# Kernel optimization log

Hardware: AMD Instinct MI355X
Metric: run time of the kernel (lower is better)

Reference implementation:

```python
import jax, jax.numpy as jnp
import numpy as np

B, T, E, H = 4, 4096, 1024, 64

def setup_inputs() -> dict:
    key = jax.random.key(0)
    k1, k2, k3, k4 = jax.random.split(key, 4)
    embeddings = jax.random.normal(k1, (B, T, E), dtype=jnp.float32)
    Wq = jax.random.normal(k2, (H, E), dtype=jnp.float32) * (1.0 / np.sqrt(E))
    Wk = jax.random.normal(k3, (H, E), dtype=jnp.float32) * (1.0 / np.sqrt(E))
    Wv = jax.random.normal(k4, (H, E), dtype=jnp.float32) * (1.0 / np.sqrt(E))
    return {"embeddings": embeddings, "Wq": Wq, "Wk": Wk, "Wv": Wv}

def reference(embeddings, Wq, Wk, Wv):
    # Linear(E, H, bias=False): x @ W.T, W: [H, E]
    q = jnp.einsum('bte,he->bth', embeddings, Wq)  # [B,T,H]
    k = jnp.einsum('bte,he->bth', embeddings, Wk)  # [B,T,H]
    v = jnp.einsum('bte,he->bth', embeddings, Wv)  # [B,T,H]
    scale = embeddings.shape[-1] ** -0.5  # NOTE: source scales by embed_size**-0.5
    wei = jnp.einsum('bqh,bkh->bqk', q, k) * scale  # [B,T,T]
    Tn = embeddings.shape[1]
    causal = jnp.tril(jnp.ones((Tn, Tn), dtype=bool))
    wei = jnp.where(causal[None, :, :], wei, -jnp.inf)
    wei = jax.nn.softmax(wei, axis=-1)
    return jnp.einsum('bqk,bkh->bqh', wei, v)  # [B,T,H]
```

## Files before the change

kernel.cpp:

```cpp
#include <hip/hip_runtime.h>
#include <math.h>
#include <stdint.h>

#define BN 4
#define TN 4096
#define EN 1024
#define HN 64
#define BT (BN*TN)

typedef __attribute__((ext_vector_type(8))) short   short8;
typedef __attribute__((ext_vector_type(4))) float   f32x4;
typedef __attribute__((ext_vector_type(4))) unsigned short us4;
typedef __attribute__((ext_vector_type(8))) unsigned short us8;

__device__ __forceinline__ unsigned short f2b(float f) {
    union { float f; uint32_t u; } v; v.f = f;
    uint32_t u = v.u;
    return (unsigned short)((u + 0x7FFFu + ((u >> 16) & 1u)) >> 16);
}

__device__ __forceinline__ float fexp2(float x) {
#if __has_builtin(__builtin_amdgcn_exp2f)
    return __builtin_amdgcn_exp2f(x);
#else
    return exp2f(x);
#endif
}

__global__ __launch_bounds__(256)
void wconv(const float* __restrict__ Wq, const float* __restrict__ Wk,
           const float* __restrict__ Wv, unsigned short* __restrict__ W16) {
    const int row = blockIdx.x;
    const int t = threadIdx.x;
    const float* src;
    float sc = 1.0f;
    if (row < 64)       { src = Wq + (size_t)row * EN; sc = 0.045084220f; }
    else if (row < 128) { src = Wk + (size_t)(row - 64) * EN; }
    else                { src = Wv + (size_t)(row - 128) * EN; }
    float4 v = *(const float4*)(src + t * 4);
    us4 p;
    p[0] = f2b(v.x * sc); p[1] = f2b(v.y * sc);
    p[2] = f2b(v.z * sc); p[3] = f2b(v.w * sc);
    *(us4*)&W16[(size_t)row * EN + t * 4] = p;
}

__global__ __launch_bounds__(512, 2)
void qkv_gemm(const float* __restrict__ emb, const unsigned short* __restrict__ W16,
              unsigned short* __restrict__ QK, unsigned short* __restrict__ VT) {
    __shared__ __align__(16) unsigned short A_lds[2][64][72];
    __shared__ __align__(16) unsigned short B_lds[2][192][72];

    const int tid = threadIdx.x;
    const int wid = tid >> 6, lane = tid & 63;
    const int c = lane & 15, g = lane >> 4;
    const int wm = wid & 1, wn = wid >> 1;
    const int r0 = blockIdx.x * 64;

    const int ar = tid >> 3, ach = tid & 7;

    const f32x4 fzero = {0.f, 0.f, 0.f, 0.f};
    f32x4 acc[2][3];
    #pragma unroll
    for (int i = 0; i < 2; ++i)
        #pragma unroll
        for (int j = 0; j < 3; ++j) acc[i][j] = fzero;

    {
        float4 a0 = *(const float4*)&emb[(size_t)(r0 + ar) * EN + ach * 8];
        float4 a1 = *(const float4*)&emb[(size_t)(r0 + ar) * EN + ach * 8 + 4];
        us8 ap;
        ap[0] = f2b(a0.x); ap[1] = f2b(a0.y); ap[2] = f2b(a0.z); ap[3] = f2b(a0.w);
        ap[4] = f2b(a1.x); ap[5] = f2b(a1.y); ap[6] = f2b(a1.z); ap[7] = f2b(a1.w);
        *(us8*)&A_lds[0][ar][ach * 8] = ap;
        #pragma unroll
        for (int s = 0; s < 3; ++s) {
            const int f = tid + 512 * s;
            const int br = f >> 3, bch = f & 7;
            *(us8*)&B_lds[0][br][bch * 8] = *(const us8*)&W16[(size_t)br * EN + bch * 8];
        }
    }
    __syncthreads();

    for (int t = 0; t < 16; ++t) {
        const int cur = t & 1;
        const bool pf = (t < 15);
        const int kn = (t + 1) * 64;

        float4 a0, a1;
        us8 bw0, bw1, bw2;
        if (pf) {
            a0 = *(const float4*)&emb[(size_t)(r0 + ar) * EN + kn + ach * 8];
            a1 = *(const float4*)&emb[(size_t)(r0 + ar) * EN + kn + ach * 8 + 4];
            bw0 = *(const us8*)&W16[(size_t)((tid +    0) >> 3) * EN + kn + (tid & 7) * 8];
            bw1 = *(const us8*)&W16[(size_t)((tid +  512) >> 3) * EN + kn + ((tid + 512) & 7) * 8];
            bw2 = *(const us8*)&W16[(size_t)((tid + 1024) >> 3) * EN + kn + ((tid + 1024) & 7) * 8];
        }

        short8 af[2][2], bf[3][2];
        #pragma unroll
        for (int rt = 0; rt < 2; ++rt)
            #pragma unroll
            for (int ks = 0; ks < 2; ++ks)
                af[rt][ks] = *(const short8*)&A_lds[cur][32 * wm + 16 * rt + c][32 * ks + 8 * g];
        #pragma unroll
        for (int nt = 0; nt < 3; ++nt)
            #pragma unroll
            for (int ks = 0; ks < 2; ++ks)
                bf[nt][ks] = *(const short8*)&B_lds[cur][48 * wn + 16 * nt + c][32 * ks + 8 * g];
        #pragma unroll
        for (int ks = 0; ks < 2; ++ks)
            #pragma unroll
            for (int rt = 0; rt < 2; ++rt)
                #pragma unroll
                for (int nt = 0; nt < 3; ++nt)
                    acc[rt][nt] = __builtin_amdgcn_mfma_f32_16x16x32_bf16(
                        af[rt][ks], bf[nt][ks], acc[rt][nt], 0, 0, 0);

        if (pf) {
            us8 ap;
            ap[0] = f2b(a0.x); ap[1] = f2b(a0.y); ap[2] = f2b(a0.z); ap[3] = f2b(a0.w);
            ap[4] = f2b(a1.x); ap[5] = f2b(a1.y); ap[6] = f2b(a1.z); ap[7] = f2b(a1.w);
            *(us8*)&A_lds[cur ^ 1][ar][ach * 8] = ap;
            *(us8*)&B_lds[cur ^ 1][(tid +    0) >> 3][((tid +    0) & 7) * 8] = bw0;
            *(us8*)&B_lds[cur ^ 1][(tid +  512) >> 3][((tid +  512) & 7) * 8] = bw1;
            *(us8*)&B_lds[cur ^ 1][(tid + 1024) >> 3][((tid + 1024) & 7) * 8] = bw2;
        }
        __syncthreads();
    }

    #pragma unroll
    for (int rt = 0; rt < 2; ++rt) {
        #pragma unroll
        for (int nt = 0; nt < 3; ++nt) {
            const int n = 48 * wn + 16 * nt + c;
            const int wsel = n >> 6;
            const int d = n & 63;
            const int rbase = r0 + 32 * wm + 16 * rt + 4 * g;
            if (wsel < 2) {
                #pragma unroll
                for (int j = 0; j < 4; ++j)
                    QK[(size_t)wsel * BT * HN + (size_t)(rbase + j) * HN + d] =
                        f2b(acc[rt][nt][j]);
            } else {
                const int bb = rbase >> 12;
                const int tt = rbase & 4095;
                us4 p;
                #pragma unroll
                for (int j = 0; j < 4; ++j) p[j] = f2b(acc[rt][nt][j]);
                *(us4*)&VT[(size_t)bb * HN * TN + (size_t)d * TN + tt] = p;
            }
        }
    }
}

#define NW 4

__global__ __launch_bounds__(256, 2)
void attn(const unsigned short* __restrict__ QK,
          const unsigned short* __restrict__ VT, float* __restrict__ out) {
    __shared__ __align__(16) unsigned short KV[NW][2][64][72];
    __shared__ __align__(16) float MLm[NW][32];
    __shared__ __align__(16) float MLl[NW][32];
    __shared__ __align__(16) float ML2m[32];
    __shared__ __align__(16) float ML2l[32];

    const int tid = threadIdx.x;
    const int w = tid >> 6, lane = tid & 63, c = lane & 15, g = lane >> 4;
    const int bid = blockIdx.x;
    const int b = bid & 3;
    const int qt = (TN / 32 - 1) - (bid >> 2);

    const unsigned short* Qg = QK + ((size_t)b * TN + (size_t)qt * 32) * HN;
    const unsigned short* Kg = QK + (size_t)BT * HN + (size_t)b * TN * HN;
    const unsigned short* Vg = VT + (size_t)b * HN * TN;

    short8 bq[2][2];
    #pragma unroll
    for (int ct = 0; ct < 2; ++ct)
        #pragma unroll
        for (int ks = 0; ks < 2; ++ks)
            bq[ct][ks] = *(const short8*)&Qg[(size_t)(16 * ct + c) * HN + 32 * ks + 8 * g];

    const f32x4 fzero = {0.f, 0.f, 0.f, 0.f};
    f32x4 o[2][4];
    #pragma unroll
    for (int i = 0; i < 2; ++i)
        #pragma unroll
        for (int j = 0; j < 4; ++j) o[i][j] = fzero;
    float m[2] = {-INFINITY, -INFINITY};
    float l[2] = {0.f, 0.f};

    const int jmax = qt >> 1;
    unsigned short* Ks = &KV[w][0][0][0];
    unsigned short* Vs = &KV[w][1][0][0];

    for (int jt = w; jt <= jmax; jt += NW) {
        #pragma unroll
        for (int i = 0; i < 8; ++i) {
            const int f = lane + 64 * i;
            const int r = f >> 3, ch = f & 7;
            *(us8*)&Ks[r * 72 + ch * 8] =
                *(const us8*)&Kg[((size_t)jt * 64 + r) * HN + ch * 8];
        }
        #pragma unroll
        for (int i = 0; i < 8; ++i) {
            const int f = lane + 64 * i;
            const int r = f >> 3, ch = f & 7;
            *(us8*)&Vs[r * 72 + ch * 8] =
                *(const us8*)&Vg[(size_t)r * TN + (size_t)jt * 64 + ch * 8];
        }

        f32x4 st[4][2];
        #pragma unroll
        for (int kt = 0; kt < 4; ++kt)
            #pragma unroll
            for (int ct = 0; ct < 2; ++ct) st[kt][ct] = fzero;
        #pragma unroll
        for (int kt = 0; kt < 4; ++kt) {
            #pragma unroll
            for (int ks = 0; ks < 2; ++ks) {
                short8 ak = *(const short8*)&Ks[(16 * kt + c) * 72 + 32 * ks + 8 * g];
                #pragma unroll
                for (int ct = 0; ct < 2; ++ct)
                    st[kt][ct] = __builtin_amdgcn_mfma_f32_16x16x32_bf16(
                        ak, bq[ct][ks], st[kt][ct], 0, 0, 0);
            }
        }

        if (jt == jmax) {
            const int koff = jt * 64 - qt * 32;
            #pragma unroll
            for (int kt = 0; kt < 4; ++kt)
                #pragma unroll
                for (int ct = 0; ct < 2; ++ct)
                    #pragma unroll
                    for (int j = 0; j < 4; ++j)
                        if (16 * kt + 4 * g + j + koff > 16 * ct + c)
                            st[kt][ct][j] = -INFINITY;
        }

        #pragma unroll
        for (int ct = 0; ct < 2; ++ct) {
            float pmax = -INFINITY;
            #pragma unroll
            for (int kt = 0; kt < 4; ++kt)
                #pragma unroll
                for (int j = 0; j < 4; ++j) pmax = fmaxf(pmax, st[kt][ct][j]);
            pmax = fmaxf(pmax, __shfl_xor(pmax, 16));
            pmax = fmaxf(pmax, __shfl_xor(pmax, 32));
            const float mn = fmaxf(m[ct], pmax);
            const float alpha = fexp2(m[ct] - mn);
            float ls = 0.f;
            #pragma unroll
            for (int kt = 0; kt < 4; ++kt)
                #pragma unroll
                for (int j = 0; j < 4; ++j) {
                    float p = fexp2(st[kt][ct][j] - mn);
                    st[kt][ct][j] = p;
                    ls += p;
                }
            ls += __shfl_xor(ls, 16);
            ls += __shfl_xor(ls, 32);
            l[ct] = l[ct] * alpha + ls;
            m[ct] = mn;

            float a4[4];
            #pragma unroll
            for (int j = 0; j < 4; ++j) a4[j] = __shfl(alpha, 4 * g + j);
            #pragma unroll
            for (int dt = 0; dt < 4; ++dt)
                #pragma unroll
                for (int j = 0; j < 4; ++j) o[ct][dt][j] *= a4[j];
        }

        #pragma unroll
        for (int kt = 0; kt < 4; ++kt)
            #pragma unroll
            for (int ct = 0; ct < 2; ++ct) {
                us4 p;
                #pragma unroll
                for (int j = 0; j < 4; ++j) p[j] = f2b(st[kt][ct][j]);
                *(us4*)&Ks[(16 * ct + c) * 72 + 16 * kt + 4 * g] = p;
            }

        #pragma unroll
        for (int ks = 0; ks < 2; ++ks) {
            short8 pa[2];
            #pragma unroll
            for (int qp = 0; qp < 2; ++qp)
                pa[qp] = *(const short8*)&Ks[(16 * qp + c) * 72 + 32 * ks + 8 * g];
            #pragma unroll
            for (int dt = 0; dt < 4; ++dt) {
                short8 bv = *(const short8*)&Vs[(16 * dt + c) * 72 + 32 * ks + 8 * g];
                #pragma unroll
                for (int qp = 0; qp < 2; ++qp)
                    o[qp][dt] = __builtin_amdgcn_mfma_f32_16x16x32_bf16(
                        pa[qp], bv, o[qp][dt], 0, 0, 0);
            }
        }
    }

    if (g == 0) {
        MLm[w][c]      = m[0];  MLl[w][c]      = l[0];
        MLm[w][c + 16] = m[1];  MLl[w][c + 16] = l[1];
    }
    __syncthreads();

    if (tid < 32) {
        const int q = tid;
        float M = MLm[0][q];
        #pragma unroll
        for (int s = 1; s < NW; ++s) M = fmaxf(M, MLm[s][q]);
        float L = 0.f;
        #pragma unroll
        for (int s = 0; s < NW; ++s) L += MLl[s][q] * fexp2(MLm[s][q] - M);
        ML2m[q] = M;
        ML2l[q] = L;
    }
    __syncthreads();

    float* Oslab = (float*)&KV[0][0][0][0];
    float* Ow = Oslab + w * (32 * 65);
    #pragma unroll
    for (int qp = 0; qp < 2; ++qp) {
        float mo[4];
        #pragma unroll
        for (int j = 0; j < 4; ++j) mo[j] = __shfl(m[qp], 4 * g + j);
        #pragma unroll
        for (int j = 0; j < 4; ++j) {
            const int q = 16 * qp + 4 * g + j;
            const float sc = fexp2(mo[j] - ML2m[q]);
            #pragma unroll
            for (int dt = 0; dt < 4; ++dt)
                Ow[q * 65 + 16 * dt + c] = o[qp][dt][j] * sc;
        }
    }
    __syncthreads();

    const int d = 16 * w + c;
    #pragma unroll
    for (int tq = 0; tq < 8; ++tq) {
        const int q = 4 * tq + g;
        float v = 0.f;
        #pragma unroll
        for (int s = 0; s < NW; ++s) v += Oslab[s * (32 * 65) + q * 65 + d];
        out[((size_t)b * TN + (size_t)qt * 32 + q) * HN + d] = v / ML2l[q];
    }
}

extern "C" void kernel_launch(void* const* d_in, const int* in_sizes, int n_in,
                              void* d_out, int out_size, void* d_ws, size_t ws_size,
                              hipStream_t stream) {
    const float* emb = (const float*)d_in[0];
    const float* Wq  = (const float*)d_in[1];
    const float* Wk  = (const float*)d_in[2];
    const float* Wv  = (const float*)d_in[3];
    float* out = (float*)d_out;

    unsigned short* ws  = (unsigned short*)d_ws;
    unsigned short* W16 = ws;
    unsigned short* QK  = ws + 196608;
    unsigned short* VT  = ws + 196608 + 2 * (size_t)BT * HN;

    wconv<<<192, 256, 0, stream>>>(Wq, Wk, Wv, W16);
    qkv_gemm<<<BT / 64, 512, 0, stream>>>(emb, W16, QK, VT);
    attn<<<BN * (TN / 32), 256, 0, stream>>>(QK, VT, out);
}
```

Before: 144.2 us.

## Deepen GEMM prefetch, double attention waves, read K/V fragments directly

The QKV GEMM now keeps two K-steps of global loads in flight in register double buffers, with the loop unrolled by two, instead of one. The attention kernel goes from 4 to 8 waves per block, splitting the key tiles across more waves. It drops the per-wave LDS staging of K and V and loads MFMA operand fragments straight from global memory; LDS is kept only for the P tile and the final cross-wave reduction. This cuts LDS traffic and footprint so more blocks can be resident, at the cost of uncoalesced global fragment loads, a larger cross-wave merge and higher register pressure.

```diff
diff --git a/kernel.cpp b/kernel.cpp
--- a/kernel.cpp
+++ b/kernel.cpp
@@ -55,8 +55,11 @@
     const int c = lane & 15, g = lane >> 4;
     const int wm = wid & 1, wn = wid >> 1;
     const int r0 = blockIdx.x * 64;
-
     const int ar = tid >> 3, ach = tid & 7;
+
+    const int br0 = tid >> 3,           bch0 = tid & 7;
+    const int br1 = (tid + 512) >> 3,   bch1 = bch0;
+    const int br2 = (tid + 1024) >> 3,  bch2 = bch0;
 
     const f32x4 fzero = {0.f, 0.f, 0.f, 0.f};
     f32x4 acc[2][3];
@@ -65,35 +68,39 @@
         #pragma unroll
         for (int j = 0; j < 3; ++j) acc[i][j] = fzero;
 
+    float4 pa0[2], pa1[2];
+    us8 pb0[2], pb1[2], pb2[2];
+
+    #pragma unroll
+    for (int t = 0; t < 2; ++t) {
+        const int k0 = t * 64;
+        pa0[t] = *(const float4*)&emb[(size_t)(r0 + ar) * EN + k0 + ach * 8];
+        pa1[t] = *(const float4*)&emb[(size_t)(r0 + ar) * EN + k0 + ach * 8 + 4];
+        pb0[t] = *(const us8*)&W16[(size_t)br0 * EN + k0 + bch0 * 8];
+        pb1[t] = *(const us8*)&W16[(size_t)br1 * EN + k0 + bch1 * 8];
+        pb2[t] = *(const us8*)&W16[(size_t)br2 * EN + k0 + bch2 * 8];
+    }
     {
-        float4 a0 = *(const float4*)&emb[(size_t)(r0 + ar) * EN + ach * 8];
-        float4 a1 = *(const float4*)&emb[(size_t)(r0 + ar) * EN + ach * 8 + 4];
         us8 ap;
-        ap[0] = f2b(a0.x); ap[1] = f2b(a0.y); ap[2] = f2b(a0.z); ap[3] = f2b(a0.w);
-        ap[4] = f2b(a1.x); ap[5] = f2b(a1.y); ap[6] = f2b(a1.z); ap[7] = f2b(a1.w);
+        ap[0] = f2b(pa0[0].x); ap[1] = f2b(pa0[0].y); ap[2] = f2b(pa0[0].z); ap[3] = f2b(pa0[0].w);
+        ap[4] = f2b(pa1[0].x); ap[5] = f2b(pa1[0].y); ap[6] = f2b(pa1[0].z); ap[7] = f2b(pa1[0].w);
         *(us8*)&A_lds[0][ar][ach * 8] = ap;
-        #pragma unroll
-        for (int s = 0; s < 3; ++s) {
-            const int f = tid + 512 * s;
-            const int br = f >> 3, bch = f & 7;
-            *(us8*)&B_lds[0][br][bch * 8] = *(const us8*)&W16[(size_t)br * EN + bch * 8];
-        }
+        *(us8*)&B_lds[0][br0][bch0 * 8] = pb0[0];
+        *(us8*)&B_lds[0][br1][bch1 * 8] = pb1[0];
+        *(us8*)&B_lds[0][br2][bch2 * 8] = pb2[0];
     }
     __syncthreads();
 
+    #pragma unroll 2
     for (int t = 0; t < 16; ++t) {
         const int cur = t & 1;
-        const bool pf = (t < 15);
-        const int kn = (t + 1) * 64;
-
-        float4 a0, a1;
-        us8 bw0, bw1, bw2;
-        if (pf) {
-            a0 = *(const float4*)&emb[(size_t)(r0 + ar) * EN + kn + ach * 8];
-            a1 = *(const float4*)&emb[(size_t)(r0 + ar) * EN + kn + ach * 8 + 4];
-            bw0 = *(const us8*)&W16[(size_t)((tid +    0) >> 3) * EN + kn + (tid & 7) * 8];
-            bw1 = *(const us8*)&W16[(size_t)((tid +  512) >> 3) * EN + kn + ((tid + 512) & 7) * 8];
-            bw2 = *(const us8*)&W16[(size_t)((tid + 1024) >> 3) * EN + kn + ((tid + 1024) & 7) * 8];
+        if (t + 2 < 16) {
+            const int kn = (t + 2) * 64;
+            pa0[cur] = *(const float4*)&emb[(size_t)(r0 + ar) * EN + kn + ach * 8];
+            pa1[cur] = *(const float4*)&emb[(size_t)(r0 + ar) * EN + kn + ach * 8 + 4];
+            pb0[cur] = *(const us8*)&W16[(size_t)br0 * EN + kn + bch0 * 8];
+            pb1[cur] = *(const us8*)&W16[(size_t)br1 * EN + kn + bch1 * 8];
+            pb2[cur] = *(const us8*)&W16[(size_t)br2 * EN + kn + bch2 * 8];
         }
 
         short8 af[2][2], bf[3][2];
@@ -116,14 +123,15 @@
                     acc[rt][nt] = __builtin_amdgcn_mfma_f32_16x16x32_bf16(
                         af[rt][ks], bf[nt][ks], acc[rt][nt], 0, 0, 0);
 
-        if (pf) {
+        if (t + 1 < 16) {
+            const int nb = cur ^ 1;
             us8 ap;
-            ap[0] = f2b(a0.x); ap[1] = f2b(a0.y); ap[2] = f2b(a0.z); ap[3] = f2b(a0.w);
-            ap[4] = f2b(a1.x); ap[5] = f2b(a1.y); ap[6] = f2b(a1.z); ap[7] = f2b(a1.w);
-            *(us8*)&A_lds[cur ^ 1][ar][ach * 8] = ap;
-            *(us8*)&B_lds[cur ^ 1][(tid +    0) >> 3][((tid +    0) & 7) * 8] = bw0;
-            *(us8*)&B_lds[cur ^ 1][(tid +  512) >> 3][((tid +  512) & 7) * 8] = bw1;
-            *(us8*)&B_lds[cur ^ 1][(tid + 1024) >> 3][((tid + 1024) & 7) * 8] = bw2;
+            ap[0] = f2b(pa0[nb].x); ap[1] = f2b(pa0[nb].y); ap[2] = f2b(pa0[nb].z); ap[3] = f2b(pa0[nb].w);
+            ap[4] = f2b(pa1[nb].x); ap[5] = f2b(pa1[nb].y); ap[6] = f2b(pa1[nb].z); ap[7] = f2b(pa1[nb].w);
+            *(us8*)&A_lds[nb][ar][ach * 8] = ap;
+            *(us8*)&B_lds[nb][br0][bch0 * 8] = pb0[nb];
+            *(us8*)&B_lds[nb][br1][bch1 * 8] = pb1[nb];
+            *(us8*)&B_lds[nb][br2][bch2 * 8] = pb2[nb];
         }
         __syncthreads();
     }
@@ -153,12 +161,12 @@
     }
 }
 
-#define NW 4
-
-__global__ __launch_bounds__(256, 2)
+#define NW 8
+
+__global__ __launch_bounds__(512, 4)
 void attn(const unsigned short* __restrict__ QK,
           const unsigned short* __restrict__ VT, float* __restrict__ out) {
-    __shared__ __align__(16) unsigned short KV[NW][2][64][72];
+    __shared__ __align__(16) unsigned char SLAB[NW * 32 * 65 * 4];
     __shared__ __align__(16) float MLm[NW][32];
     __shared__ __align__(16) float MLl[NW][32];
     __shared__ __align__(16) float ML2m[32];
@@ -174,6 +182,8 @@
     const unsigned short* Kg = QK + (size_t)BT * HN + (size_t)b * TN * HN;
     const unsigned short* Vg = VT + (size_t)b * HN * TN;
 
+    unsigned short* Pw = (unsigned short*)SLAB + (size_t)w * 32 * 72;
+
     short8 bq[2][2];
     #pragma unroll
     for (int ct = 0; ct < 2; ++ct)
@@ -191,25 +201,8 @@
     float l[2] = {0.f, 0.f};
 
     const int jmax = qt >> 1;
-    unsigned short* Ks = &KV[w][0][0][0];
-    unsigned short* Vs = &KV[w][1][0][0];
 
     for (int jt = w; jt <= jmax; jt += NW) {
-        #pragma unroll
-        for (int i = 0; i < 8; ++i) {
-            const int f = lane + 64 * i;
-            const int r = f >> 3, ch = f & 7;
-            *(us8*)&Ks[r * 72 + ch * 8] =
-                *(const us8*)&Kg[((size_t)jt * 64 + r) * HN + ch * 8];
-        }
-        #pragma unroll
-        for (int i = 0; i < 8; ++i) {
-            const int f = lane + 64 * i;
-            const int r = f >> 3, ch = f & 7;
-            *(us8*)&Vs[r * 72 + ch * 8] =
-                *(const us8*)&Vg[(size_t)r * TN + (size_t)jt * 64 + ch * 8];
-        }
-
         f32x4 st[4][2];
         #pragma unroll
         for (int kt = 0; kt < 4; ++kt)
@@ -219,7 +212,8 @@
         for (int kt = 0; kt < 4; ++kt) {
             #pragma unroll
             for (int ks = 0; ks < 2; ++ks) {
-                short8 ak = *(const short8*)&Ks[(16 * kt + c) * 72 + 32 * ks + 8 * g];
+                short8 ak = *(const short8*)
+                    &Kg[((size_t)jt * 64 + 16 * kt + c) * HN + 32 * ks + 8 * g];
                 #pragma unroll
                 for (int ct = 0; ct < 2; ++ct)
                     st[kt][ct] = __builtin_amdgcn_mfma_f32_16x16x32_bf16(
@@ -280,7 +274,7 @@
                 us4 p;
                 #pragma unroll
                 for (int j = 0; j < 4; ++j) p[j] = f2b(st[kt][ct][j]);
-                *(us4*)&Ks[(16 * ct + c) * 72 + 16 * kt + 4 * g] = p;
+                *(us4*)&Pw[(16 * ct + c) * 72 + 16 * kt + 4 * g] = p;
             }
 
         #pragma unroll
@@ -288,10 +282,11 @@
             short8 pa[2];
             #pragma unroll
             for (int qp = 0; qp < 2; ++qp)
-                pa[qp] = *(const short8*)&Ks[(16 * qp + c) * 72 + 32 * ks + 8 * g];
+                pa[qp] = *(const short8*)&Pw[(16 * qp + c) * 72 + 32 * ks + 8 * g];
             #pragma unroll
             for (int dt = 0; dt < 4; ++dt) {
-                short8 bv = *(const short8*)&Vs[(16 * dt + c) * 72 + 32 * ks + 8 * g];
+                short8 bv = *(const short8*)
+                    &Vg[(size_t)(16 * dt + c) * TN + jt * 64 + 32 * ks + 8 * g];
                 #pragma unroll
                 for (int qp = 0; qp < 2; ++qp)
                     o[qp][dt] = __builtin_amdgcn_mfma_f32_16x16x32_bf16(
@@ -319,8 +314,8 @@
     }
     __syncthreads();
 
-    float* Oslab = (float*)&KV[0][0][0][0];
-    float* Ow = Oslab + w * (32 * 65);
+    float* Oslab = (float*)SLAB;
+    float* Ow = Oslab + (size_t)w * (32 * 65);
     #pragma unroll
     for (int qp = 0; qp < 2; ++qp) {
         float mo[4];
@@ -337,13 +332,14 @@
     }
     __syncthreads();
 
-    const int d = 16 * w + c;
-    #pragma unroll
-    for (int tq = 0; tq < 8; ++tq) {
-        const int q = 4 * tq + g;
+    const int d = 16 * (w & 3) + c;
+    const int qb = 16 * (w >> 2);
+    #pragma unroll
+    for (int j = 0; j < 4; ++j) {
+        const int q = qb + 4 * g + j;
         float v = 0.f;
         #pragma unroll
-        for (int s = 0; s < NW; ++s) v += Oslab[s * (32 * 65) + q * 65 + d];
+        for (int s = 0; s < NW; ++s) v += Oslab[(size_t)s * (32 * 65) + q * 65 + d];
         out[((size_t)b * TN + (size_t)qt * 32 + q) * HN + d] = v / ML2l[q];
     }
 }
@@ -364,5 +360,5 @@
 
     wconv<<<192, 256, 0, stream>>>(Wq, Wk, Wv, W16);
     qkv_gemm<<<BT / 64, 512, 0, stream>>>(emb, W16, QK, VT);
-    attn<<<BN * (TN / 32), 256, 0, stream>>>(QK, VT, out);
-}
+    attn<<<BN * (TN / 32), 512, 0, stream>>>(QK, VT, out);
+}
```

After: 163.8 us. 1.14x slower.
